# Kernel optimization log

Measured on AMD Instinct MI355X. Metric: run time of the kernel, lower is better.

The kernel has to match this reference:

```python
import jax, jax.numpy as jnp
import numpy as np

B, S, HID = 2, 2048, 2048
NH, NKV, HD = 32, 8, 64
ROPE_THETA = 10000.0
SCALE = HD ** -0.5


def _rope_cos_sin(seq_len, head_dim, theta):
    inv_freq = 1.0 / (theta ** (jnp.arange(0, head_dim, 2, dtype=jnp.float32) / head_dim))
    pos = jnp.arange(seq_len, dtype=jnp.float32)
    freqs = jnp.outer(pos, inv_freq)              # [S, HD/2]
    emb = jnp.concatenate([freqs, freqs], axis=-1)  # [S, HD]
    return jnp.cos(emb), jnp.sin(emb)


def _rotate_half(x):
    x1, x2 = jnp.split(x, 2, axis=-1)
    return jnp.concatenate([-x2, x1], axis=-1)


def setup_inputs() -> dict:
    key = jax.random.key(0)
    ks = jax.random.split(key, 8)
    s = 0.02
    return {
        "hidden_states": jax.random.normal(ks[0], (B, S, HID), jnp.float32),
        "q_w": jax.random.normal(ks[1], (NH * HD, HID), jnp.float32) * s,
        "q_b": jax.random.normal(ks[2], (NH * HD,), jnp.float32) * s,
        "k_w": jax.random.normal(ks[3], (NKV * HD, HID), jnp.float32) * s,
        "k_b": jax.random.normal(ks[4], (NKV * HD,), jnp.float32) * s,
        "v_w": jax.random.normal(ks[5], (NKV * HD, HID), jnp.float32) * s,
        "v_b": jax.random.normal(ks[6], (NKV * HD,), jnp.float32) * s,
        "o_w": jax.random.normal(ks[7], (HID, NH * HD), jnp.float32) * s,
    }


def reference(hidden_states, q_w, q_b, k_w, k_b, v_w, v_b, o_w):
    bsz, q_len, _ = hidden_states.shape
    # QKV projections (nn.Linear: x @ W^T + b)
    q = hidden_states @ q_w.T + q_b   # [B, S, NH*HD]
    k = hidden_states @ k_w.T + k_b   # [B, S, NKV*HD]
    v = hidden_states @ v_w.T + v_b
    # reshape to [B, H, S, D]
    q = q.reshape(bsz, q_len, NH, HD).transpose(0, 2, 1, 3)
    k = k.reshape(bsz, q_len, NKV, HD).transpose(0, 2, 1, 3)
    v = v.reshape(bsz, q_len, NKV, HD).transpose(0, 2, 1, 3)
    # RoPE
    cos, sin = _rope_cos_sin(q_len, HD, ROPE_THETA)  # [S, HD]
    cos = cos[None, None]; sin = sin[None, None]
    q = q * cos + _rotate_half(q) * sin
    k = k * cos + _rotate_half(k) * sin
    # GQA: expand kv heads to match query heads
    groups = NH // NKV
    k = jnp.repeat(k, groups, axis=1)  # [B, NH, S, D]
    v = jnp.repeat(v, groups, axis=1)
    # scaled dot-product attention with causal mask
    scores = jnp.einsum('bhqd,bhkd->bhqk', q, k) * SCALE
    causal = jnp.tril(jnp.ones((q_len, q_len), dtype=bool))
    scores = jnp.where(causal[None, None], scores, jnp.finfo(scores.dtype).min)
    probs = jax.nn.softmax(scores, axis=-1)
    out = jnp.einsum('bhqk,bhkd->bhqd', probs, v)  # [B, NH, S, D]
    out = out.transpose(0, 2, 1, 3).reshape(bsz, q_len, NH * HD)
    return out @ o_w.T  # [B, S, HID]
```

## Files before the change

kernel.cpp:

```cpp
#include <hip/hip_runtime.h>
#include <stdint.h>
#include <stddef.h>

typedef __attribute__((ext_vector_type(8))) short s16x8;
typedef __attribute__((ext_vector_type(4))) short s16x4;
typedef __attribute__((ext_vector_type(4))) float f32x4;

#define S_LEN 2048
#define HID 2048
#define QKV_N 3072
#define NHEAD 32
#define NKVH 8

__device__ __forceinline__ unsigned short f2bf(float f) {
  union { float f; unsigned u; } a; a.f = f;
  unsigned u = a.u;
  u += 0x7fffu + ((u >> 16) & 1u);
  return (unsigned short)(u >> 16);
}
__device__ __forceinline__ float bf2f(unsigned short h) {
  union { unsigned u; float f; } a; a.u = ((unsigned)h) << 16;
  return a.f;
}
__device__ __forceinline__ void gl_lds16(const unsigned short* g, short* l) {
  __builtin_amdgcn_global_load_lds(
      (const __attribute__((address_space(1))) unsigned int*)g,
      (__attribute__((address_space(3))) unsigned int*)l, 16, 0, 0);
}

__global__ void k_convert(const float* __restrict__ x, const float* __restrict__ wq,
                          const float* __restrict__ wk, const float* __restrict__ wv,
                          const float* __restrict__ wo, unsigned short* __restrict__ dst) {
  const unsigned n4 = 18874368u / 4u;
  for (unsigned i = blockIdx.x * blockDim.x + threadIdx.x; i < n4;
       i += gridDim.x * blockDim.x) {
    unsigned e = i * 4u;
    const float* src; unsigned off;
    if (e < 8388608u)       { src = x;  off = e; }
    else if (e < 12582912u) { src = wq; off = e - 8388608u; }
    else if (e < 13631488u) { src = wk; off = e - 12582912u; }
    else if (e < 14680064u) { src = wv; off = e - 13631488u; }
    else                    { src = wo; off = e - 14680064u; }
    f32x4 v = *(const f32x4*)(src + off);
    s16x4 o;
    o[0] = (short)f2bf(v[0]); o[1] = (short)f2bf(v[1]);
    o[2] = (short)f2bf(v[2]); o[3] = (short)f2bf(v[3]);
    *(s16x4*)(dst + e) = o;
  }
}

__global__ void k_rope_table(float* __restrict__ cost, float* __restrict__ sint) {
  int idx = blockIdx.x * 256 + threadIdx.x;
  int i = idx & 31, s = idx >> 5;
  float inv = powf(10000.0f, -(float)(2 * i) / 64.0f);
  float ang = (float)s * inv;
  cost[idx] = cosf(ang);
  sint[idx] = sinf(ang);
}

template <int MODE>
__global__ __launch_bounds__(256) void k_gemm(
    const unsigned short* __restrict__ A,
    const unsigned short* __restrict__ W0, const unsigned short* __restrict__ W1,
    const unsigned short* __restrict__ W2,
    const float* __restrict__ b0, const float* __restrict__ b1, const float* __restrict__ b2,
    unsigned short* __restrict__ Cb, float* __restrict__ Cf) {
  __shared__ short lA[128 * 32];
  __shared__ short lB[128 * 32];
  const int K = 2048;
  int tid = threadIdx.x;
  int wave = tid >> 6, lane = tid & 63;
  int l15 = lane & 15, lg = lane >> 4;
  int tn = blockIdx.x, tm = blockIdx.y;
  const unsigned short* W; const float* bias = nullptr; int col0;
  if constexpr (MODE == 0) {
    if (tn < 16)      { W = W0; bias = b0; col0 = tn * 128; }
    else if (tn < 20) { W = W1; bias = b1; col0 = (tn - 16) * 128; }
    else              { W = W2; bias = b2; col0 = (tn - 20) * 128; }
  } else { W = W0; col0 = tn * 128; }
  int m0 = tm * 128;
  int wm = wave >> 1, wn = wave & 1;

  const unsigned short* gA0 = A + (size_t)(m0 + (tid >> 2)) * K + (tid & 3) * 8;
  const unsigned short* gA1 = gA0 + (size_t)64 * K;
  const unsigned short* gB0 = W + (size_t)(col0 + (tid >> 2)) * K + (tid & 3) * 8;
  const unsigned short* gB1 = gB0 + (size_t)64 * K;
  short* sA0 = &lA[wave * 512];
  short* sA1 = &lA[2048 + wave * 512];
  short* sB0 = &lB[wave * 512];
  short* sB1 = &lB[2048 + wave * 512];

  f32x4 acc[4][4];
#pragma unroll
  for (int m = 0; m < 4; ++m)
#pragma unroll
    for (int n = 0; n < 4; ++n) acc[m][n] = (f32x4){0.f, 0.f, 0.f, 0.f};

  for (int kt = 0; kt < K; kt += 32) {
    __syncthreads();
    gl_lds16(gA0 + kt, sA0);
    gl_lds16(gA1 + kt, sA1);
    gl_lds16(gB0 + kt, sB0);
    gl_lds16(gB1 + kt, sB1);
    asm volatile("s_waitcnt vmcnt(0)" ::: "memory");
    __syncthreads();
    s16x8 af[4], bfr[4];
    const short* pa = &lA[(wm * 64 + l15) * 32 + lg * 8];
    const short* pb = &lB[(wn * 64 + l15) * 32 + lg * 8];
#pragma unroll
    for (int m = 0; m < 4; ++m) af[m] = *(const s16x8*)(pa + m * 512);
#pragma unroll
    for (int n = 0; n < 4; ++n) bfr[n] = *(const s16x8*)(pb + n * 512);
#pragma unroll
    for (int m = 0; m < 4; ++m)
#pragma unroll
      for (int n = 0; n < 4; ++n)
        acc[m][n] = __builtin_amdgcn_mfma_f32_16x16x32_bf16(af[m], bfr[n], acc[m][n], 0, 0, 0);
  }

#pragma unroll
  for (int n = 0; n < 4; ++n) {
    int lcol = col0 + wn * 64 + n * 16 + l15;
    int gcol = tn * 128 + wn * 64 + n * 16 + l15;
    float bv = 0.f;
    if constexpr (MODE == 0) bv = bias[lcol];
#pragma unroll
    for (int m = 0; m < 4; ++m) {
      int row = m0 + wm * 64 + m * 16 + lg * 4;
#pragma unroll
      for (int r = 0; r < 4; ++r) {
        float v = acc[m][n][r] + bv;
        if constexpr (MODE == 0)
          Cb[(size_t)(row + r) * QKV_N + gcol] = f2bf(v);
        else
          Cf[(size_t)(row + r) * HID + gcol] = v;
      }
    }
  }
}

__global__ void k_rope_apply(unsigned short* __restrict__ qkv,
                             const float* __restrict__ cost, const float* __restrict__ sint) {
  int t = blockIdx.x * blockDim.x + threadIdx.x;
  int chunk = t & 3;
  int head = (t >> 2) % 40;
  int row = t / 160;
  int colb = head < 32 ? head * 64 : 2048 + (head - 32) * 64;
  int d0 = chunk * 8;
  int s = row & (S_LEN - 1);
  unsigned short* p = qkv + (size_t)row * QKV_N + colb;
  s16x8 lo = *(s16x8*)(p + d0);
  s16x8 hi = *(s16x8*)(p + 32 + d0);
  const float* cb = cost + s * 32 + d0;
  const float* sb = sint + s * 32 + d0;
  f32x4 c0 = *(const f32x4*)cb, c1 = *(const f32x4*)(cb + 4);
  f32x4 s0 = *(const f32x4*)sb, s1 = *(const f32x4*)(sb + 4);
  float cc[8] = {c0[0], c0[1], c0[2], c0[3], c1[0], c1[1], c1[2], c1[3]};
  float ss[8] = {s0[0], s0[1], s0[2], s0[3], s1[0], s1[1], s1[2], s1[3]};
  s16x8 nlo, nhi;
#pragma unroll
  for (int j = 0; j < 8; ++j) {
    float xl = bf2f((unsigned short)lo[j]);
    float xh = bf2f((unsigned short)hi[j]);
    nlo[j] = (short)f2bf(xl * cc[j] - xh * ss[j]);
    nhi[j] = (short)f2bf(xh * cc[j] + xl * ss[j]);
  }
  *(s16x8*)(p + d0) = nlo;
  *(s16x8*)(p + 32 + d0) = nhi;
}

__global__ void k_vtrans(const unsigned short* __restrict__ qkv, unsigned short* __restrict__ vt) {
  __shared__ unsigned short t[64][80];
  int ts = blockIdx.x & 63, td = blockIdx.x >> 6;
  int tid = threadIdx.x;
#pragma unroll
  for (int L = 0; L < 2; ++L) {
    int c = L * 256 + tid;
    int row = c >> 3, ch = c & 7;
    const unsigned short* src = qkv + (size_t)(ts * 64 + row) * QKV_N + 2560 + td * 64 + ch * 8;
    s16x8 v = *(const s16x8*)src;
    int cs = (ch * 8) ^ ((row >> 3) << 3);
    *(s16x8*)&t[row][cs] = v;
  }
  __syncthreads();
  int b = (ts * 64) >> 11;
  int s0 = (ts * 64) & (S_LEN - 1);
#pragma unroll
  for (int L = 0; L < 2; ++L) {
    int c = L * 256 + tid;
    int d = c >> 3, sc = c & 7;
    s16x8 o;
#pragma unroll
    for (int j = 0; j < 8; ++j) o[j] = (short)t[sc * 8 + j][d ^ (sc << 3)];
    unsigned short* dst = vt + ((size_t)((b * 8 + td) * 64 + d)) * 2048 + s0 + sc * 8;
    *(s16x8*)dst = o;
  }
}

__global__ __launch_bounds__(512, 4) void k_attn(const unsigned short* __restrict__ qkv,
                                                 const unsigned short* __restrict__ vt,
                                                 unsigned short* __restrict__ aout) {
  __shared__ unsigned short lK[2][4096];
  __shared__ unsigned short lV[2][4096];
  __shared__ unsigned short pl[8][2048];
  int wave = threadIdx.x >> 6, lane = threadIdx.x & 63;
  int l15 = lane & 15, lg = lane >> 4;
  int bi = blockIdx.x;
  int ip = bi >> 4;
  int b  = (bi >> 3) & 1;
  int hg = bi & 7;
  int wgrp = wave >> 2;
  int wh = wave & 3;
  int h = hg * 4 + wh;
  int t = wgrp ? ip : (63 - ip);
  int q0 = t * 32;
  int kbend = t >> 1;
  int kbmaxB = (63 - ip) >> 1;

  const unsigned short* qb_ = qkv + (size_t)(b * S_LEN) * QKV_N + h * 64;
  const unsigned short* kbase = qkv + (size_t)(b * S_LEN) * QKV_N + 2048 + hg * 64;
  const unsigned short* vbase = vt + (size_t)((b * NKVH + hg) * 64) * 2048;
  unsigned short* pw = &pl[wave][0];
  int sw = (l15 & 7) << 3;

  int srow = wave * 8 + (lane >> 3);
  int ssw = 8 * ((lane & 7) ^ ((lane >> 3) & 7));
  const unsigned short* gk0 = kbase + (size_t)srow * QKV_N + ssw;
  const unsigned short* gv0 = vbase + (size_t)srow * 2048 + ssw;
  short* lkd0 = (short*)&lK[0][wave * 512]; short* lkd1 = (short*)&lK[1][wave * 512];
  short* lvd0 = (short*)&lV[0][wave * 512]; short* lvd1 = (short*)&lV[1][wave * 512];

  s16x8 aq[2][2];
#pragma unroll
  for (int m = 0; m < 2; ++m)
#pragma unroll
    for (int ks = 0; ks < 2; ++ks)
      aq[m][ks] = *(const s16x8*)(qb_ + (size_t)(q0 + m * 16 + l15) * QKV_N + ks * 32 + lg * 8);

  f32x4 acc[2][4];
  float mrow[2], lrow[2];
#pragma unroll
  for (int m = 0; m < 2; ++m) {
#pragma unroll
    for (int dt = 0; dt < 4; ++dt) acc[m][dt] = (f32x4){0.f, 0.f, 0.f, 0.f};
    mrow[m] = -3.0e38f; lrow[m] = 0.f;
  }

  gl_lds16(gk0, lkd0);
  gl_lds16(gv0, lvd0);
  asm volatile("s_waitcnt vmcnt(0)" ::: "memory");
  __syncthreads();

  for (int kb = 0; kb <= kbmaxB; ++kb) {
    const unsigned short* lk = &lK[kb & 1][0];
    const unsigned short* lv = &lV[kb & 1][0];
    if (kb < kbmaxB) {
      size_t go = (size_t)(kb + 1) * 64;
      if ((kb & 1) == 0) { gl_lds16(gk0 + go * QKV_N, lkd1); gl_lds16(gv0 + go, lvd1); }
      else               { gl_lds16(gk0 + go * QKV_N, lkd0); gl_lds16(gv0 + go, lvd0); }
    }
    if (kb <= kbend) {
      bool need_mask = (kb == kbend);
#pragma unroll
      for (int m = 0; m < 2; ++m) {
        f32x4 z[4];
        __builtin_amdgcn_s_setprio(1);
#pragma unroll
        for (int nt = 0; nt < 4; ++nt) {
          s16x8 k0 = *(const s16x8*)(lk + (nt * 16 + l15) * 64 + ((lg * 8) ^ sw));
          s16x8 k1 = *(const s16x8*)(lk + (nt * 16 + l15) * 64 + ((32 + lg * 8) ^ sw));
          f32x4 zz = (f32x4){0.f, 0.f, 0.f, 0.f};
          zz = __builtin_amdgcn_mfma_f32_16x16x32_bf16(k0, aq[m][0], zz, 0, 0, 0);
          zz = __builtin_amdgcn_mfma_f32_16x16x32_bf16(k1, aq[m][1], zz, 0, 0, 0);
          z[nt] = zz;
        }
        __builtin_amdgcn_s_setprio(0);
        float s[16];
        int q = q0 + m * 16 + l15;
#pragma unroll
        for (int nt = 0; nt < 4; ++nt)
#pragma unroll
          for (int r = 0; r < 4; ++r) {
            float v = z[nt][r] * 0.125f;
            if (need_mask) {
              int k = kb * 64 + nt * 16 + lg * 4 + r;
              if (k > q) v = -3.0e38f;
            }
            s[nt * 4 + r] = v;
          }
        float mx = s[0];
#pragma unroll
        for (int i = 1; i < 16; ++i) mx = fmaxf(mx, s[i]);
        mx = fmaxf(mx, __shfl_xor(mx, 16));
        mx = fmaxf(mx, __shfl_xor(mx, 32));
        float nm = fmaxf(mrow[m], mx);
        float corr = __expf(mrow[m] - nm);
        mrow[m] = nm;
        float rs = 0.f;
#pragma unroll
        for (int nt = 0; nt < 4; ++nt) {
          s16x4 pk;
#pragma unroll
          for (int r = 0; r < 4; ++r) {
            float p = __expf(s[nt * 4 + r] - nm);
            rs += p;
            pk[r] = (short)f2bf(p);
          }
          *(s16x4*)(pw + (m * 16 + l15) * 64 + ((nt * 16 + lg * 4) ^ sw)) = pk;
        }
        rs += __shfl_xor(rs, 16);
        rs += __shfl_xor(rs, 32);
        lrow[m] = lrow[m] * corr + rs;
#pragma unroll
        for (int r = 0; r < 4; ++r) {
          float cr = __shfl(corr, lg * 4 + r);
#pragma unroll
          for (int dt = 0; dt < 4; ++dt) acc[m][dt][r] *= cr;
        }
      }
      s16x8 pa[2][2];
#pragma unroll
      for (int m = 0; m < 2; ++m)
#pragma unroll
        for (int ks = 0; ks < 2; ++ks)
          pa[m][ks] = *(const s16x8*)(pw + (m * 16 + l15) * 64 + ((ks * 32 + lg * 8) ^ sw));
      __builtin_amdgcn_s_setprio(1);
#pragma unroll
      for (int dt = 0; dt < 4; ++dt) {
        s16x8 v0 = *(const s16x8*)(lv + (dt * 16 + l15) * 64 + ((lg * 8) ^ sw));
        s16x8 v1 = *(const s16x8*)(lv + (dt * 16 + l15) * 64 + ((32 + lg * 8) ^ sw));
#pragma unroll
        for (int m = 0; m < 2; ++m) {
          acc[m][dt] = __builtin_amdgcn_mfma_f32_16x16x32_bf16(pa[m][0], v0, acc[m][dt], 0, 0, 0);
          acc[m][dt] = __builtin_amdgcn_mfma_f32_16x16x32_bf16(pa[m][1], v1, acc[m][dt], 0, 0, 0);
        }
      }
      __builtin_amdgcn_s_setprio(0);
    }
    asm volatile("s_waitcnt vmcnt(0)" ::: "memory");
    __syncthreads();
  }

  unsigned short* ob = aout + (size_t)(b * S_LEN) * HID + h * 64;
#pragma unroll
  for (int m = 0; m < 2; ++m)
#pragma unroll
    for (int r = 0; r < 4; ++r) {
      float lr = __shfl(lrow[m], lg * 4 + r);
      float inv = 1.0f / lr;
#pragma unroll
      for (int dt = 0; dt < 4; ++dt)
        ob[(size_t)(q0 + m * 16 + lg * 4 + r) * HID + dt * 16 + l15] = f2bf(acc[m][dt][r] * inv);
    }
}

extern "C" void kernel_launch(void* const* d_in, const int* in_sizes, int n_in,
                              void* d_out, int out_size, void* d_ws, size_t ws_size,
                              hipStream_t stream) {
  const float* x  = (const float*)d_in[0];
  const float* qw = (const float*)d_in[1];
  const float* qb = (const float*)d_in[2];
  const float* kw = (const float*)d_in[3];
  const float* kbias = (const float*)d_in[4];
  const float* vw = (const float*)d_in[5];
  const float* vbias = (const float*)d_in[6];
  const float* ow = (const float*)d_in[7];

  unsigned short* Xb  = (unsigned short*)d_ws;
  unsigned short* Wqb = Xb + 8388608;
  unsigned short* Wkb = Wqb + 4194304;
  unsigned short* Wvb = Wkb + 1048576;
  unsigned short* Wob = Wvb + 1048576;
  unsigned short* QKV = Wob + 4194304;
  unsigned short* VT  = QKV + 12582912;
  unsigned short* AO  = VT + 2097152;
  float* COS = (float*)(AO + 8388608);
  float* SIN = COS + 65536;

  k_convert<<<1024, 256, 0, stream>>>(x, qw, kw, vw, ow, Xb);
  k_rope_table<<<256, 256, 0, stream>>>(COS, SIN);
  k_gemm<0><<<dim3(24, 32), 256, 0, stream>>>(Xb, Wqb, Wkb, Wvb, qb, kbias, vbias, QKV, nullptr);
  k_rope_apply<<<2560, 256, 0, stream>>>(QKV, COS, SIN);
  k_vtrans<<<512, 256, 0, stream>>>(QKV, VT);
  k_attn<<<512, 512, 0, stream>>>(QKV, VT, AO);
  k_gemm<1><<<dim3(16, 32), 256, 0, stream>>>(AO, Wob, nullptr, nullptr,
                                              nullptr, nullptr, nullptr, nullptr, (float*)d_out);
}
```

Baseline: 227.5 us.

## Fuse RoPE into QKV GEMM epilogue and use lazy rescaling exp2 softmax

Removes the separate RoPE kernel by applying the rotation in the QKV GEMM epilogue, which pairs accumulator column tiles n and n+2 (d and d+32). This saves a full read-modify-write pass over Q and K. The attention softmax now folds log2(e) into the scale and uses exp2. It skips the running-max rescale unless some row's max grows by more than 8 (log2 units), and packs probabilities to bf16 with a hardware cvt_pk instruction. The lazy rescale bounds unnormalized values by 2^8, which adds some precision risk.

```diff
diff --git a/kernel.cpp b/kernel.cpp
--- a/kernel.cpp
+++ b/kernel.cpp
@@ -5,6 +5,7 @@
 typedef __attribute__((ext_vector_type(8))) short s16x8;
 typedef __attribute__((ext_vector_type(4))) short s16x4;
 typedef __attribute__((ext_vector_type(4))) float f32x4;
+typedef __attribute__((ext_vector_type(2))) unsigned int u32x2;
 
 #define S_LEN 2048
 #define HID 2048
@@ -21,6 +22,11 @@
 __device__ __forceinline__ float bf2f(unsigned short h) {
   union { unsigned u; float f; } a; a.u = ((unsigned)h) << 16;
   return a.f;
+}
+__device__ __forceinline__ unsigned cvt_pk_bf16(float a, float b) {
+  unsigned r;
+  asm("v_cvt_pk_bf16_f32 %0, %1, %2" : "=v"(r) : "v"(a), "v"(b));
+  return r;
 }
 __device__ __forceinline__ void gl_lds16(const unsigned short* g, short* l) {
   __builtin_amdgcn_global_load_lds(
@@ -64,6 +70,7 @@
     const unsigned short* __restrict__ W0, const unsigned short* __restrict__ W1,
     const unsigned short* __restrict__ W2,
     const float* __restrict__ b0, const float* __restrict__ b1, const float* __restrict__ b2,
+    const float* __restrict__ ct, const float* __restrict__ st,
     unsigned short* __restrict__ Cb, float* __restrict__ Cf) {
   __shared__ short lA[128 * 32];
   __shared__ short lB[128 * 32];
@@ -118,55 +125,46 @@
         acc[m][n] = __builtin_amdgcn_mfma_f32_16x16x32_bf16(af[m], bfr[n], acc[m][n], 0, 0, 0);
   }
 
-#pragma unroll
-  for (int n = 0; n < 4; ++n) {
-    int lcol = col0 + wn * 64 + n * 16 + l15;
-    int gcol = tn * 128 + wn * 64 + n * 16 + l15;
-    float bv = 0.f;
-    if constexpr (MODE == 0) bv = bias[lcol];
-#pragma unroll
-    for (int m = 0; m < 4; ++m) {
-      int row = m0 + wm * 64 + m * 16 + lg * 4;
-#pragma unroll
-      for (int r = 0; r < 4; ++r) {
-        float v = acc[m][n][r] + bv;
-        if constexpr (MODE == 0)
-          Cb[(size_t)(row + r) * QKV_N + gcol] = f2bf(v);
-        else
-          Cf[(size_t)(row + r) * HID + gcol] = v;
+  if constexpr (MODE == 0) {
+    bool rope = (tn < 20);
+#pragma unroll
+    for (int n = 0; n < 2; ++n) {
+      int lcol = col0 + wn * 64 + n * 16 + l15;
+      int gcol = tn * 128 + wn * 64 + n * 16 + l15;
+      float blo = bias[lcol], bhi = bias[lcol + 32];
+      int i = n * 16 + l15;
+#pragma unroll
+      for (int m = 0; m < 4; ++m) {
+        int row = m0 + wm * 64 + m * 16 + lg * 4;
+#pragma unroll
+        for (int r = 0; r < 4; ++r) {
+          float xl = acc[m][n][r] + blo;
+          float xh = acc[m][n + 2][r] + bhi;
+          if (rope) {
+            int s = (row + r) & (S_LEN - 1);
+            float c = ct[s * 32 + i], sn = st[s * 32 + i];
+            float nl = xl * c - xh * sn;
+            xh = xh * c + xl * sn;
+            xl = nl;
+          }
+          Cb[(size_t)(row + r) * QKV_N + gcol] = f2bf(xl);
+          Cb[(size_t)(row + r) * QKV_N + gcol + 32] = f2bf(xh);
+        }
       }
     }
-  }
-}
-
-__global__ void k_rope_apply(unsigned short* __restrict__ qkv,
-                             const float* __restrict__ cost, const float* __restrict__ sint) {
-  int t = blockIdx.x * blockDim.x + threadIdx.x;
-  int chunk = t & 3;
-  int head = (t >> 2) % 40;
-  int row = t / 160;
-  int colb = head < 32 ? head * 64 : 2048 + (head - 32) * 64;
-  int d0 = chunk * 8;
-  int s = row & (S_LEN - 1);
-  unsigned short* p = qkv + (size_t)row * QKV_N + colb;
-  s16x8 lo = *(s16x8*)(p + d0);
-  s16x8 hi = *(s16x8*)(p + 32 + d0);
-  const float* cb = cost + s * 32 + d0;
-  const float* sb = sint + s * 32 + d0;
-  f32x4 c0 = *(const f32x4*)cb, c1 = *(const f32x4*)(cb + 4);
-  f32x4 s0 = *(const f32x4*)sb, s1 = *(const f32x4*)(sb + 4);
-  float cc[8] = {c0[0], c0[1], c0[2], c0[3], c1[0], c1[1], c1[2], c1[3]};
-  float ss[8] = {s0[0], s0[1], s0[2], s0[3], s1[0], s1[1], s1[2], s1[3]};
-  s16x8 nlo, nhi;
-#pragma unroll
-  for (int j = 0; j < 8; ++j) {
-    float xl = bf2f((unsigned short)lo[j]);
-    float xh = bf2f((unsigned short)hi[j]);
-    nlo[j] = (short)f2bf(xl * cc[j] - xh * ss[j]);
-    nhi[j] = (short)f2bf(xh * cc[j] + xl * ss[j]);
-  }
-  *(s16x8*)(p + d0) = nlo;
-  *(s16x8*)(p + 32 + d0) = nhi;
+  } else {
+#pragma unroll
+    for (int n = 0; n < 4; ++n) {
+      int gcol = tn * 128 + wn * 64 + n * 16 + l15;
+#pragma unroll
+      for (int m = 0; m < 4; ++m) {
+        int row = m0 + wm * 64 + m * 16 + lg * 4;
+#pragma unroll
+        for (int r = 0; r < 4; ++r)
+          Cf[(size_t)(row + r) * HID + gcol] = acc[m][n][r];
+      }
+    }
+  }
 }
 
 __global__ void k_vtrans(const unsigned short* __restrict__ qkv, unsigned short* __restrict__ vt) {
@@ -246,6 +244,8 @@
     mrow[m] = -3.0e38f; lrow[m] = 0.f;
   }
 
+  const float CSC = 0.125f * 1.44269504f;
+
   gl_lds16(gk0, lkd0);
   gl_lds16(gv0, lvd0);
   asm volatile("s_waitcnt vmcnt(0)" ::: "memory");
@@ -281,42 +281,50 @@
         for (int nt = 0; nt < 4; ++nt)
 #pragma unroll
           for (int r = 0; r < 4; ++r) {
-            float v = z[nt][r] * 0.125f;
+            float v = z[nt][r] * CSC;
             if (need_mask) {
               int k = kb * 64 + nt * 16 + lg * 4 + r;
-              if (k > q) v = -3.0e38f;
+              if (k > q) v = -1.0e30f;
             }
             s[nt * 4 + r] = v;
           }
-        float mx = s[0];
-#pragma unroll
-        for (int i = 1; i < 16; ++i) mx = fmaxf(mx, s[i]);
+        float m01 = fmaxf(s[0], s[1]), m23 = fmaxf(s[2], s[3]);
+        float m45 = fmaxf(s[4], s[5]), m67 = fmaxf(s[6], s[7]);
+        float m89 = fmaxf(s[8], s[9]), mab = fmaxf(s[10], s[11]);
+        float mcd = fmaxf(s[12], s[13]), mef = fmaxf(s[14], s[15]);
+        float mx = fmaxf(fmaxf(fmaxf(m01, m23), fmaxf(m45, m67)),
+                         fmaxf(fmaxf(m89, mab), fmaxf(mcd, mef)));
         mx = fmaxf(mx, __shfl_xor(mx, 16));
         mx = fmaxf(mx, __shfl_xor(mx, 32));
-        float nm = fmaxf(mrow[m], mx);
-        float corr = __expf(mrow[m] - nm);
-        mrow[m] = nm;
+        if (!__all(mx <= mrow[m] + 8.0f)) {
+          float nm = fmaxf(mrow[m], mx);
+          float corr = __builtin_amdgcn_exp2f(mrow[m] - nm);
+          mrow[m] = nm;
+          lrow[m] *= corr;
+#pragma unroll
+          for (int r = 0; r < 4; ++r) {
+            float cr = __shfl(corr, lg * 4 + r);
+#pragma unroll
+            for (int dt = 0; dt < 4; ++dt) acc[m][dt][r] *= cr;
+          }
+        }
+        float nm = mrow[m];
         float rs = 0.f;
 #pragma unroll
         for (int nt = 0; nt < 4; ++nt) {
-          s16x4 pk;
-#pragma unroll
-          for (int r = 0; r < 4; ++r) {
-            float p = __expf(s[nt * 4 + r] - nm);
-            rs += p;
-            pk[r] = (short)f2bf(p);
-          }
-          *(s16x4*)(pw + (m * 16 + l15) * 64 + ((nt * 16 + lg * 4) ^ sw)) = pk;
+          float p0 = __builtin_amdgcn_exp2f(s[nt * 4 + 0] - nm);
+          float p1 = __builtin_amdgcn_exp2f(s[nt * 4 + 1] - nm);
+          float p2 = __builtin_amdgcn_exp2f(s[nt * 4 + 2] - nm);
+          float p3 = __builtin_amdgcn_exp2f(s[nt * 4 + 3] - nm);
+          rs += (p0 + p1) + (p2 + p3);
+          u32x2 w;
+          w[0] = cvt_pk_bf16(p0, p1);
+          w[1] = cvt_pk_bf16(p2, p3);
+          *(u32x2*)(pw + (m * 16 + l15) * 64 + ((nt * 16 + lg * 4) ^ sw)) = w;
         }
         rs += __shfl_xor(rs, 16);
         rs += __shfl_xor(rs, 32);
-        lrow[m] = lrow[m] * corr + rs;
-#pragma unroll
-        for (int r = 0; r < 4; ++r) {
-          float cr = __shfl(corr, lg * 4 + r);
-#pragma unroll
-          for (int dt = 0; dt < 4; ++dt) acc[m][dt][r] *= cr;
-        }
+        lrow[m] += rs;
       }
       s16x8 pa[2][2];
 #pragma unroll
@@ -379,10 +387,11 @@
 
   k_convert<<<1024, 256, 0, stream>>>(x, qw, kw, vw, ow, Xb);
   k_rope_table<<<256, 256, 0, stream>>>(COS, SIN);
-  k_gemm<0><<<dim3(24, 32), 256, 0, stream>>>(Xb, Wqb, Wkb, Wvb, qb, kbias, vbias, QKV, nullptr);
-  k_rope_apply<<<2560, 256, 0, stream>>>(QKV, COS, SIN);
+  k_gemm<0><<<dim3(24, 32), 256, 0, stream>>>(Xb, Wqb, Wkb, Wvb, qb, kbias, vbias,
+                                              COS, SIN, QKV, nullptr);
   k_vtrans<<<512, 256, 0, stream>>>(QKV, VT);
   k_attn<<<512, 512, 0, stream>>>(QKV, VT, AO);
   k_gemm<1><<<dim3(16, 32), 256, 0, stream>>>(AO, Wob, nullptr, nullptr,
-                                              nullptr, nullptr, nullptr, nullptr, (float*)d_out);
-}
+                                              nullptr, nullptr, nullptr, nullptr, nullptr,
+                                              nullptr, (float*)d_out);
+}
```

New measurement: 208.6 us. -8.3%, faster.
